# Kernel optimization log

Hardware: AMD Instinct MI355X
Metric: run time of the kernel (lower is better)

Reference implementation:

```python
import jax, jax.numpy as jnp
import numpy as np

DIM = 768
H = 12
D = DIM // H  # head_dim = 64
SCALE = D ** -0.5


def _split_heads(x):
    # [b, n, h*d] -> [b, h, n, d]
    b, n, _ = x.shape
    return x.reshape(b, n, H, D).transpose(0, 2, 1, 3)


def setup_inputs() -> dict:
    key = jax.random.key(0)
    ks = jax.random.split(key, 16)
    B, NQ, NKV = 2, 2048, 2048
    w_init = lambda k: jax.random.normal(k, (DIM, DIM), dtype=jnp.float32) * 0.02
    return {
        "words": jax.random.normal(ks[0], (B, NQ, DIM), dtype=jnp.float32),
        "position_words": jax.random.normal(ks[1], (B, NQ, DIM), dtype=jnp.float32),
        "conscious_words": jax.random.normal(ks[2], (B, NQ, DIM), dtype=jnp.float32),
        "cross_kv": jax.random.normal(ks[3], (B, NKV, DIM), dtype=jnp.float32),
        "position_cross": jax.random.normal(ks[4], (B, NKV, DIM), dtype=jnp.float32),
        "Wq_w": w_init(ks[5]), "Wk_w": w_init(ks[6]), "Wv_w": w_init(ks[7]),
        "Wq_p": w_init(ks[8]), "Wk_p": w_init(ks[9]),
        "Wq_c": w_init(ks[10]), "Wk_c": w_init(ks[11]),
        "latent_k": jax.random.normal(ks[12], (DIM,), dtype=jnp.float32),
        "Wo": w_init(ks[13]),
        "bo": jnp.zeros((DIM,), dtype=jnp.float32),
    }


def reference(words, position_words, conscious_words, cross_kv, position_cross,
              Wq_w, Wk_w, Wv_w, Wq_p, Wk_p, Wq_c, Wk_c, latent_k, Wo, bo):
    # Queries from three sources. Sum of the 9 pairwise QK^T scores equals
    # (sum of Qs) @ (sum of Ks)^T by bilinearity of matmul (same math as source).
    q = _split_heads(words @ Wq_w) + _split_heads(position_words @ Wq_p) \
        + _split_heads(conscious_words @ Wq_c)        # [b,h,nq,d]
    # latent conscious key: same vector for every kv position
    kc = (latent_k @ Wk_c).reshape(H, D)              # [h,d]
    k = _split_heads(cross_kv @ Wk_w) + _split_heads(position_cross @ Wk_p) \
        + kc[None, :, None, :]                        # [b,h,nkv,d]
    v = _split_heads(cross_kv @ Wv_w)                 # [b,h,nkv,d]

    score = jnp.einsum('bhid,bhjd->bhij', q, k) * SCALE  # [b,h,nq,nkv]
    attn = jax.nn.softmax(score, axis=-1)
    out = jnp.einsum('bhij,bhjd->bhid', attn, v)      # [b,h,nq,d]
    b, _, nq, _ = out.shape
    out = out.transpose(0, 2, 1, 3).reshape(b, nq, H * D)
    return out @ Wo + bo
```

## Files before the change

kernel.cpp:

```cpp
#include <hip/hip_runtime.h>
#include <math.h>

#define DIM  768
#define NH   12
#define HD   64
#define NQ   2048
#define NKV  2048
#define QSC_LOG2E 0.18033688011112042f

typedef short bf16x8  __attribute__((ext_vector_type(8)));
typedef float f32x4   __attribute__((ext_vector_type(4)));
typedef float f32x16  __attribute__((ext_vector_type(16)));

__device__ __forceinline__ unsigned short f2bf(float f) {
    unsigned u = __float_as_uint(f);
    unsigned r = (u + 0x7FFFu + ((u >> 16) & 1u)) >> 16;
    return (unsigned short)r;
}

__device__ __forceinline__ unsigned cvtpk_bf16(float a, float b) {
    unsigned r;
    asm("v_cvt_pk_bf16_f32 %0, %1, %2" : "=v"(r) : "v"(a), "v"(b));
    return r;
}

__device__ __forceinline__ void plswap(unsigned& a, unsigned& b) {
    asm("v_permlane32_swap_b32 %0, %1" : "+v"(a), "+v"(b));
}

__device__ __forceinline__ float vexp2f(float x) {
#if __has_builtin(__builtin_amdgcn_exp2f)
    return __builtin_amdgcn_exp2f(x);
#else
    float r;
    asm("v_exp_f32 %0, %1\ns_nop 0" : "=v"(r) : "v"(x));
    return r;
#endif
}

__device__ __forceinline__ void ld_lds16(void* lds, const void* g) {
    __builtin_amdgcn_global_load_lds(
        (const __attribute__((address_space(1))) unsigned int*)g,
        (__attribute__((address_space(3))) unsigned int*)lds, 16, 0, 0);
}

__device__ __forceinline__ f32x16 z16() {
    f32x16 r;
    #pragma unroll
    for (int e = 0; e < 16; ++e) r[e] = 0.f;
    return r;
}

union PB16 { unsigned u[4]; bf16x8 v; };

__global__ __launch_bounds__(256)
void kc2_kernel(const float* __restrict__ latent, const float* __restrict__ Wkc,
                float* __restrict__ kc) {
    __shared__ float red[16][17];
    int tx = threadIdx.x & 15, ty = threadIdx.x >> 4;
    int j = blockIdx.x * 16 + tx;
    float acc = 0.f;
    for (int i = ty * 48; i < ty * 48 + 48; ++i) acc += latent[i] * Wkc[i * DIM + j];
    red[ty][tx] = acc;
    __syncthreads();
    if (ty == 0) {
        float s = 0.f;
        #pragma unroll
        for (int k = 0; k < 16; ++k) s += red[k][tx];
        kc[j] = s;
    }
}

__global__ __launch_bounds__(256)
void convert_acts(const float* __restrict__ s0, const float* __restrict__ s1,
                  const float* __restrict__ s2, const float* __restrict__ s3,
                  const float* __restrict__ s4,
                  unsigned short* __restrict__ dstA, unsigned short* __restrict__ dstB) {
    const float* srcs[5] = {s0, s1, s2, s3, s4};
    int y = blockIdx.y;
    const float* s = srcs[y];
    unsigned short* d = (y < 4) ? (dstA + (size_t)y * 3145728) : dstB;
    size_t i = ((size_t)blockIdx.x * 256 + threadIdx.x) * 4;
    float4 v = *(const float4*)(s + i);
    ushort4 o;
    o.x = f2bf(v.x); o.y = f2bf(v.y); o.z = f2bf(v.z); o.w = f2bf(v.w);
    *(ushort4*)(d + i) = o;
}

__global__ __launch_bounds__(256)
void conv_w(const float* __restrict__ w0, const float* __restrict__ w1,
            const float* __restrict__ w2, const float* __restrict__ w3,
            const float* __restrict__ w4, const float* __restrict__ w5,
            const float* __restrict__ w6, unsigned short* __restrict__ dst) {
    __shared__ float t[32][33];
    const float* Ws[7] = {w0, w1, w2, w3, w4, w5, w6};
    const float* W = Ws[blockIdx.z];
    unsigned short* D = dst + (size_t)blockIdx.z * (768 * 768);
    int r0 = blockIdx.y * 32, c0 = blockIdx.x * 32;
    int tx = threadIdx.x & 31, ty = threadIdx.x >> 5;
    #pragma unroll
    for (int yy = 0; yy < 4; ++yy)
        t[ty * 4 + yy][tx] = W[(size_t)(r0 + ty * 4 + yy) * 768 + c0 + tx];
    __syncthreads();
    #pragma unroll
    for (int yy = 0; yy < 4; ++yy)
        D[(size_t)(c0 + ty * 4 + yy) * 768 + r0 + tx] = f2bf(t[tx][ty * 4 + yy]);
}

template<int NPAIR, int MODE>
__global__ __launch_bounds__(256)
void mfma_gemm(const unsigned short* __restrict__ A0, const unsigned short* __restrict__ B0,
               const unsigned short* __restrict__ A1, const unsigned short* __restrict__ B1,
               const unsigned short* __restrict__ A2, const unsigned short* __restrict__ B2,
               const float* __restrict__ bias, float scale, void* __restrict__ Cout) {
    __shared__ unsigned short As[2][64 * 64];
    __shared__ unsigned short Bs[2][128 * 64];
    const int tid = threadIdx.x;
    const int w = tid >> 6, l = tid & 63, g = l >> 4, r16 = l & 15;

    int o_lin = blockIdx.x + 6 * blockIdx.y;
    int wl = (o_lin & 7) * 48 + (o_lin >> 3);
    int bx = wl % 6, by = wl / 6;
    const int n0 = bx * 128, m0 = by * 64;

    const unsigned short* Alist[3] = {A0, A1, A2};
    const unsigned short* Blist[3] = {B0, B1, B2};

    f32x4 acc[4][2];
    #pragma unroll
    for (int i = 0; i < 4; ++i)
        #pragma unroll
        for (int j = 0; j < 2; ++j) acc[i][j] = (f32x4){0.f, 0.f, 0.f, 0.f};

#define GSTAGE(BUFI, AP, BP, K0) { \
    _Pragma("unroll") \
    for (int is = 0; is < 2; ++is) { \
        int u = is * 256 + tid, r = u >> 3, cc = u & 7; \
        int col = ((cc ^ (r & 7)) << 3); \
        ld_lds16((char*)As[BUFI] + is * 4096 + w * 1024, \
                 (AP) + (size_t)(m0 + r) * 768 + (K0) + col); } \
    _Pragma("unroll") \
    for (int is = 0; is < 4; ++is) { \
        int u = is * 256 + tid, r = u >> 3, cc = u & 7; \
        int col = ((cc ^ (r & 7)) << 3); \
        ld_lds16((char*)Bs[BUFI] + is * 4096 + w * 1024, \
                 (BP) + (size_t)(n0 + r) * 768 + (K0) + col); } }

    const int NSTEPS = NPAIR * 12;
    int pn = 0, kn = 0;
    GSTAGE(0, Alist[0], Blist[0], 0);
    kn = 64; if (kn == 768) { kn = 0; ++pn; }
    __syncthreads();

    #pragma unroll 1
    for (int st = 0; st < NSTEPS; ++st) {
        int cur = st & 1;
        if (st + 1 < NSTEPS) {
            GSTAGE(cur ^ 1, Alist[pn], Blist[pn], kn);
            kn += 64; if (kn == 768) { kn = 0; ++pn; }
        }
        const char* Ab = (const char*)As[cur];
        const char* Bb = (const char*)Bs[cur];
        #pragma unroll
        for (int kk = 0; kk < 2; ++kk) {
            bf16x8 af[4], bf[2];
            #pragma unroll
            for (int i = 0; i < 4; ++i) {
                int row = i * 16 + r16;
                af[i] = *(const bf16x8*)(Ab + row * 128 +
                          ((kk * 64 + g * 16) ^ ((row & 7) << 4)));
            }
            #pragma unroll
            for (int j = 0; j < 2; ++j) {
                int row = w * 32 + j * 16 + r16;
                bf[j] = *(const bf16x8*)(Bb + row * 128 +
                          ((kk * 64 + g * 16) ^ ((row & 7) << 4)));
            }
            #pragma unroll
            for (int i = 0; i < 4; ++i)
                #pragma unroll
                for (int j = 0; j < 2; ++j)
                    acc[i][j] = __builtin_amdgcn_mfma_f32_16x16x32_bf16(
                        af[i], bf[j], acc[i][j], 0, 0, 0);
        }
        __syncthreads();
    }
#undef GSTAGE

    #pragma unroll
    for (int i = 0; i < 4; ++i) {
        #pragma unroll
        for (int j = 0; j < 2; ++j) {
            int col = n0 + w * 32 + j * 16 + r16;
            float bv = ((MODE == 0 && bias) || MODE == 1) ? bias[col] : 0.f;
            #pragma unroll
            for (int rr = 0; rr < 4; ++rr) {
                int row = m0 + i * 16 + g * 4 + rr;
                float v = acc[i][j][rr];
                if (MODE == 2) v *= scale;
                v += bv;
                if (MODE == 1) {
                    ((float*)Cout)[(size_t)row * 768 + col] = v;
                } else if (MODE == 3) {
                    int bb = row >> 11, q = row & 2047;
                    ((unsigned short*)Cout)[(size_t)(bb * 768 + col) * 2048 + q] = f2bf(v);
                } else {
                    ((unsigned short*)Cout)[(size_t)row * 768 + col] = f2bf(v);
                }
            }
        }
    }
}

__global__ __launch_bounds__(256)
void flash2(const unsigned short* __restrict__ Qb,
            const unsigned short* __restrict__ Kb,
            const unsigned short* __restrict__ Vt,
            unsigned short* __restrict__ AO) {
    __shared__ unsigned short KV[2][2][4096];
    const int tid = threadIdx.x;
    const int w = tid >> 6, l = tid & 63, lo = l & 31, hi = l >> 5;

    int o_lin = blockIdx.x + 16 * blockIdx.y;
    int wl = (o_lin & 7) * 48 + (o_lin >> 3);
    int qi = wl & 15, bh = wl >> 4;
    int b = bh / NH, h = bh % NH;
    int q0 = qi * 128;

    bf16x8 qf[4];
    {
        const unsigned short* Qrow =
            Qb + (size_t)(b * NQ + q0 + w * 32 + lo) * DIM + h * HD + hi * 8;
        #pragma unroll
        for (int kc = 0; kc < 4; ++kc) qf[kc] = *(const bf16x8*)(Qrow + kc * 16);
    }

    f32x16 o0 = z16(), o1 = z16();
    float m = -3.0e38f, lsum = 0.f;

    const unsigned short* Kbase = Kb + (size_t)(b * NKV) * DIM + h * HD;
    const unsigned short* Vbase = Vt + ((size_t)b * DIM + h * HD) * NKV;

#define FSTAGE(BUFI, T0) { \
    _Pragma("unroll") \
    for (int is = 0; is < 2; ++is) { \
        int u = is * 256 + tid, r = u >> 3, cc = u & 7; \
        int col = ((cc ^ (r & 7)) << 3); \
        ld_lds16((char*)KV[BUFI][0] + is * 4096 + w * 1024, \
                 Kbase + (size_t)((T0) + r) * 768 + col); \
        ld_lds16((char*)KV[BUFI][1] + is * 4096 + w * 1024, \
                 Vbase + (size_t)r * 2048 + (T0) + col); } }

    FSTAGE(0, 0);
    __syncthreads();

    #pragma unroll 1
    for (int t = 0; t < 32; ++t) {
        int cur = t & 1;
        if (t < 31) FSTAGE(cur ^ 1, (t + 1) * 64);

        const char* Kp = (const char*)KV[cur][0];
        const char* Vp = (const char*)KV[cur][1];

        f32x16 s0 = z16(), s1 = z16();
        #pragma unroll
        for (int kc = 0; kc < 4; ++kc) {
            int r0 = lo, r1 = 32 + lo;
            bf16x8 k0 = *(const bf16x8*)(Kp + r0 * 128 +
                          ((kc * 32 + hi * 16) ^ ((r0 & 7) << 4)));
            bf16x8 k1 = *(const bf16x8*)(Kp + r1 * 128 +
                          ((kc * 32 + hi * 16) ^ ((r1 & 7) << 4)));
            s0 = __builtin_amdgcn_mfma_f32_32x32x16_bf16(k0, qf[kc], s0, 0, 0, 0);
            s1 = __builtin_amdgcn_mfma_f32_32x32x16_bf16(k1, qf[kc], s1, 0, 0, 0);
        }

        float a8[8];
        #pragma unroll
        for (int e = 0; e < 8; ++e)
            a8[e] = fmaxf(fmaxf(s0[e], s0[e + 8]), fmaxf(s1[e], s1[e + 8]));
        #pragma unroll
        for (int e = 0; e < 4; ++e) a8[e] = fmaxf(a8[e], a8[e + 4]);
        float pm = fmaxf(fmaxf(a8[0], a8[1]), fmaxf(a8[2], a8[3]));
        pm = fmaxf(pm, __shfl_xor(pm, 32));

        if (__any(pm > m + 10.f)) {
            float mn = fmaxf(m, pm);
            float sc = vexp2f(m - mn);
            lsum *= sc;
            #pragma unroll
            for (int e = 0; e < 16; ++e) { o0[e] *= sc; o1[e] *= sc; }
            m = mn;
        }

        #pragma unroll
        for (int e = 0; e < 16; ++e) {
            s0[e] = vexp2f(s0[e] - m);
            s1[e] = vexp2f(s1[e] - m);
        }

        float b8[8];
        #pragma unroll
        for (int e = 0; e < 8; ++e)
            b8[e] = (s0[e] + s0[e + 8]) + (s1[e] + s1[e + 8]);
        float rs = ((b8[0] + b8[1]) + (b8[2] + b8[3])) +
                   ((b8[4] + b8[5]) + (b8[6] + b8[7]));
        rs += __shfl_xor(rs, 32);
        lsum += rs;

        PB16 pb[4];
        #pragma unroll
        for (int cc = 0; cc < 2; ++cc) {
            unsigned a0 = cvtpk_bf16(s0[cc * 8 + 0], s0[cc * 8 + 1]);
            unsigned a1 = cvtpk_bf16(s0[cc * 8 + 2], s0[cc * 8 + 3]);
            unsigned b0 = cvtpk_bf16(s0[cc * 8 + 4], s0[cc * 8 + 5]);
            unsigned b1 = cvtpk_bf16(s0[cc * 8 + 6], s0[cc * 8 + 7]);
            plswap(a0, b0);
            plswap(a1, b1);
            pb[cc].u[0] = a0; pb[cc].u[1] = a1; pb[cc].u[2] = b0; pb[cc].u[3] = b1;
            unsigned c0 = cvtpk_bf16(s1[cc * 8 + 0], s1[cc * 8 + 1]);
            unsigned c1 = cvtpk_bf16(s1[cc * 8 + 2], s1[cc * 8 + 3]);
            unsigned d0 = cvtpk_bf16(s1[cc * 8 + 4], s1[cc * 8 + 5]);
            unsigned d1 = cvtpk_bf16(s1[cc * 8 + 6], s1[cc * 8 + 7]);
            plswap(c0, d0);
            plswap(c1, d1);
            pb[2 + cc].u[0] = c0; pb[2 + cc].u[1] = c1;
            pb[2 + cc].u[2] = d0; pb[2 + cc].u[3] = d1;
        }

        #pragma unroll
        for (int c = 0; c < 4; ++c) {
            int r0 = lo, r1 = 32 + lo;
            bf16x8 v0 = *(const bf16x8*)(Vp + r0 * 128 +
                          ((c * 32 + hi * 16) ^ ((r0 & 7) << 4)));
            bf16x8 v1 = *(const bf16x8*)(Vp + r1 * 128 +
                          ((c * 32 + hi * 16) ^ ((r1 & 7) << 4)));
            o0 = __builtin_amdgcn_mfma_f32_32x32x16_bf16(v0, pb[c].v, o0, 0, 0, 0);
            o1 = __builtin_amdgcn_mfma_f32_32x32x16_bf16(v1, pb[c].v, o1, 0, 0, 0);
        }
        __syncthreads();
    }
#undef FSTAGE

    float inv = 1.f / lsum;
    char* eb = (char*)KV + w * 4096;
    #pragma unroll
    for (int r = 0; r < 16; r += 2) {
        int d0 = (r & 3) + 8 * (r >> 2) + 4 * hi;
        *(unsigned*)(eb + lo * 128 + ((2 * d0) ^ ((lo & 7) << 4))) =
            cvtpk_bf16(o0[r] * inv, o0[r + 1] * inv);
        int d1 = 32 + d0;
        *(unsigned*)(eb + lo * 128 + ((2 * d1) ^ ((lo & 7) << 4))) =
            cvtpk_bf16(o1[r] * inv, o1[r + 1] * inv);
    }
    int q2 = l >> 1, h2 = l & 1;
    size_t grow = (size_t)(b * NQ + q0 + w * 32 + q2) * DIM + h * HD + h2 * 32;
    #pragma unroll
    for (int c = 0; c < 4; ++c) {
        uint4 vv = *(const uint4*)(eb + q2 * 128 + ((h2 * 64 + c * 16) ^ ((q2 & 7) << 4)));
        *(uint4*)(AO + grow + c * 8) = vv;
    }
}

extern "C" void kernel_launch(void* const* d_in, const int* in_sizes, int n_in,
                              void* d_out, int out_size, void* d_ws, size_t ws_size,
                              hipStream_t stream) {
    const float* words   = (const float*)d_in[0];
    const float* posw    = (const float*)d_in[1];
    const float* consc   = (const float*)d_in[2];
    const float* cross   = (const float*)d_in[3];
    const float* pcross  = (const float*)d_in[4];
    const float* Wq_w    = (const float*)d_in[5];
    const float* Wk_w    = (const float*)d_in[6];
    const float* Wv_w    = (const float*)d_in[7];
    const float* Wq_p    = (const float*)d_in[8];
    const float* Wk_p    = (const float*)d_in[9];
    const float* Wq_c    = (const float*)d_in[10];
    const float* Wk_c    = (const float*)d_in[11];
    const float* latentk = (const float*)d_in[12];
    const float* Wo      = (const float*)d_in[13];
    const float* bo      = (const float*)d_in[14];

    char* arena = (char*)d_ws;
    const size_t ACTB = 6291456;
    unsigned short* act0 = (unsigned short*)(arena);
    unsigned short* act1 = (unsigned short*)(arena + ACTB);
    unsigned short* act2 = (unsigned short*)(arena + 2 * ACTB);
    unsigned short* act3 = (unsigned short*)(arena + 3 * ACTB);
    unsigned short* wt   = (unsigned short*)(arena + 4 * ACTB);
    const size_t WTE = 768 * 768;
    unsigned short* qb  = (unsigned short*)(arena + 4 * ACTB + 7 * WTE * 2);
    unsigned short* pcb = (unsigned short*)((char*)qb + ACTB);
    float* kcv          = (float*)((char*)pcb + ACTB);

    unsigned short* kb = act1;
    unsigned short* vt = act2;
    unsigned short* ao = act0;

    convert_acts<<<dim3(3072, 5), dim3(256), 0, stream>>>(
        words, posw, consc, cross, pcross, act0, pcb);
    conv_w<<<dim3(24, 24, 7), dim3(256), 0, stream>>>(
        Wq_w, Wq_p, Wq_c, Wk_w, Wk_p, Wv_w, Wo, wt);
    kc2_kernel<<<dim3(48), dim3(256), 0, stream>>>(latentk, Wk_c, kcv);

    mfma_gemm<3, 2><<<dim3(6, 64), dim3(256), 0, stream>>>(
        act0, wt + 0 * WTE, act1, wt + 1 * WTE, act2, wt + 2 * WTE,
        nullptr, QSC_LOG2E, qb);
    mfma_gemm<1, 3><<<dim3(6, 64), dim3(256), 0, stream>>>(
        act3, wt + 5 * WTE, nullptr, nullptr, nullptr, nullptr,
        nullptr, 1.f, vt);
    mfma_gemm<2, 0><<<dim3(6, 64), dim3(256), 0, stream>>>(
        act3, wt + 3 * WTE, pcb, wt + 4 * WTE, nullptr, nullptr,
        kcv, 1.f, kb);
    flash2<<<dim3(16, 24), dim3(256), 0, stream>>>(qb, kb, vt, ao);
    mfma_gemm<1, 1><<<dim3(6, 64), dim3(256), 0, stream>>>(
        ao, wt + 6 * WTE, nullptr, nullptr, nullptr, nullptr,
        bo, 1.f, (float*)d_out);
}
```

Before: 160.0 us.

## Split attention KV range in two with combine pass, merge Q/V projection launches

The flash attention kernel now splits each (batch, head, q-tile) over two halves of the KV sequence. That doubles the grid from 384 to 768 blocks for better CU occupancy. Each half writes unnormalized partial outputs plus running max and sum, and a new combine kernel merges them into the attention output. The Q and V projection GEMMs are fused into one launch through a runtime-configured GEMM kernel, and workspace buffers are reused. The cost is extra global traffic for the partial outputs, an extra launch, and runtime mode branches that replace template constants in the GEMM.

```diff
diff --git a/kernel.cpp b/kernel.cpp
--- a/kernel.cpp
+++ b/kernel.cpp
@@ -16,6 +16,9 @@
     unsigned u = __float_as_uint(f);
     unsigned r = (u + 0x7FFFu + ((u >> 16) & 1u)) >> 16;
     return (unsigned short)r;
+}
+__device__ __forceinline__ float bf2f(unsigned short u) {
+    return __uint_as_float(((unsigned)u) << 16);
 }
 
 __device__ __forceinline__ unsigned cvtpk_bf16(float a, float b) {
@@ -74,12 +77,11 @@
 __global__ __launch_bounds__(256)
 void convert_acts(const float* __restrict__ s0, const float* __restrict__ s1,
                   const float* __restrict__ s2, const float* __restrict__ s3,
-                  const float* __restrict__ s4,
-                  unsigned short* __restrict__ dstA, unsigned short* __restrict__ dstB) {
-    const float* srcs[5] = {s0, s1, s2, s3, s4};
+                  unsigned short* __restrict__ dstA) {
+    const float* srcs[4] = {s0, s1, s2, s3};
     int y = blockIdx.y;
     const float* s = srcs[y];
-    unsigned short* d = (y < 4) ? (dstA + (size_t)y * 3145728) : dstB;
+    unsigned short* d = dstA + (size_t)y * 3145728;
     size_t i = ((size_t)blockIdx.x * 256 + threadIdx.x) * 4;
     float4 v = *(const float4*)(s + i);
     ushort4 o;
@@ -107,24 +109,40 @@
         D[(size_t)(c0 + ty * 4 + yy) * 768 + r0 + tx] = f2bf(t[tx][ty * 4 + yy]);
 }
 
-template<int NPAIR, int MODE>
-__global__ __launch_bounds__(256)
-void mfma_gemm(const unsigned short* __restrict__ A0, const unsigned short* __restrict__ B0,
-               const unsigned short* __restrict__ A1, const unsigned short* __restrict__ B1,
-               const unsigned short* __restrict__ A2, const unsigned short* __restrict__ B2,
-               const float* __restrict__ bias, float scale, void* __restrict__ Cout) {
+struct GemmCfg {
+    const unsigned short* A0; const unsigned short* A1; const unsigned short* A2;
+    const unsigned short* B0; const unsigned short* B1; const unsigned short* B2;
+    const float* bias; float scale; void* out; int npair; int mode;
+};
+
+__global__ __launch_bounds__(256)
+void gemm_any(GemmCfg c0, GemmCfg c1, int nblk) {
     __shared__ unsigned short As[2][64 * 64];
     __shared__ unsigned short Bs[2][128 * 64];
     const int tid = threadIdx.x;
     const int w = tid >> 6, l = tid & 63, g = l >> 4, r16 = l & 15;
 
-    int o_lin = blockIdx.x + 6 * blockIdx.y;
-    int wl = (o_lin & 7) * 48 + (o_lin >> 3);
-    int bx = wl % 6, by = wl / 6;
+    int o_lin = blockIdx.x + 6 * blockIdx.y + 384 * blockIdx.z;
+    int per = nblk >> 3;
+    int wl = (o_lin & 7) * per + (o_lin >> 3);
+    int zz = wl / 384, rem = wl - zz * 384;
+    int bx = rem % 6, by = rem / 6;
     const int n0 = bx * 128, m0 = by * 64;
 
-    const unsigned short* Alist[3] = {A0, A1, A2};
-    const unsigned short* Blist[3] = {B0, B1, B2};
+    const unsigned short* Alist[3];
+    const unsigned short* Blist[3];
+    const float* bias; float scale; void* Cout; int npair, mode;
+    if (zz == 0) {
+        Alist[0] = c0.A0; Alist[1] = c0.A1; Alist[2] = c0.A2;
+        Blist[0] = c0.B0; Blist[1] = c0.B1; Blist[2] = c0.B2;
+        bias = c0.bias; scale = c0.scale; Cout = c0.out;
+        npair = c0.npair; mode = c0.mode;
+    } else {
+        Alist[0] = c1.A0; Alist[1] = c1.A1; Alist[2] = c1.A2;
+        Blist[0] = c1.B0; Blist[1] = c1.B1; Blist[2] = c1.B2;
+        bias = c1.bias; scale = c1.scale; Cout = c1.out;
+        npair = c1.npair; mode = c1.mode;
+    }
 
     f32x4 acc[4][2];
     #pragma unroll
@@ -146,10 +164,10 @@
         ld_lds16((char*)Bs[BUFI] + is * 4096 + w * 1024, \
                  (BP) + (size_t)(n0 + r) * 768 + (K0) + col); } }
 
-    const int NSTEPS = NPAIR * 12;
+    const int NSTEPS = npair * 12;
     int pn = 0, kn = 0;
     GSTAGE(0, Alist[0], Blist[0], 0);
-    kn = 64; if (kn == 768) { kn = 0; ++pn; }
+    kn = 64;
     __syncthreads();
 
     #pragma unroll 1
@@ -192,16 +210,16 @@
         #pragma unroll
         for (int j = 0; j < 2; ++j) {
             int col = n0 + w * 32 + j * 16 + r16;
-            float bv = ((MODE == 0 && bias) || MODE == 1) ? bias[col] : 0.f;
+            float bv = ((mode == 0 && bias) || mode == 1) ? bias[col] : 0.f;
             #pragma unroll
             for (int rr = 0; rr < 4; ++rr) {
                 int row = m0 + i * 16 + g * 4 + rr;
                 float v = acc[i][j][rr];
-                if (MODE == 2) v *= scale;
+                if (mode == 2) v *= scale;
                 v += bv;
-                if (MODE == 1) {
+                if (mode == 1) {
                     ((float*)Cout)[(size_t)row * 768 + col] = v;
-                } else if (MODE == 3) {
+                } else if (mode == 3) {
                     int bb = row >> 11, q = row & 2047;
                     ((unsigned short*)Cout)[(size_t)(bb * 768 + col) * 2048 + q] = f2bf(v);
                 } else {
@@ -216,16 +234,19 @@
 void flash2(const unsigned short* __restrict__ Qb,
             const unsigned short* __restrict__ Kb,
             const unsigned short* __restrict__ Vt,
-            unsigned short* __restrict__ AO) {
+            unsigned short* __restrict__ P0,
+            unsigned short* __restrict__ P1,
+            float2* __restrict__ ML) {
     __shared__ unsigned short KV[2][2][4096];
     const int tid = threadIdx.x;
     const int w = tid >> 6, l = tid & 63, lo = l & 31, hi = l >> 5;
 
-    int o_lin = blockIdx.x + 16 * blockIdx.y;
-    int wl = (o_lin & 7) * 48 + (o_lin >> 3);
-    int qi = wl & 15, bh = wl >> 4;
+    int o_lin = blockIdx.x + 32 * blockIdx.y;
+    int wl = (o_lin & 7) * 96 + (o_lin >> 3);
+    int qi = wl & 15, part = (wl >> 4) & 1, bh = wl >> 5;
     int b = bh / NH, h = bh % NH;
     int q0 = qi * 128;
+    int kvbase = part * 1024;
 
     bf16x8 qf[4];
     {
@@ -251,13 +272,13 @@
         ld_lds16((char*)KV[BUFI][1] + is * 4096 + w * 1024, \
                  Vbase + (size_t)r * 2048 + (T0) + col); } }
 
-    FSTAGE(0, 0);
+    FSTAGE(0, kvbase);
     __syncthreads();
 
     #pragma unroll 1
-    for (int t = 0; t < 32; ++t) {
+    for (int t = 0; t < 16; ++t) {
         int cur = t & 1;
-        if (t < 31) FSTAGE(cur ^ 1, (t + 1) * 64);
+        if (t < 15) FSTAGE(cur ^ 1, kvbase + (t + 1) * 64);
 
         const char* Kp = (const char*)KV[cur][0];
         const char* Vp = (const char*)KV[cur][1];
@@ -341,23 +362,46 @@
     }
 #undef FSTAGE
 
-    float inv = 1.f / lsum;
-    char* eb = (char*)KV + w * 4096;
-    #pragma unroll
-    for (int r = 0; r < 16; r += 2) {
+    unsigned short* Op = (part ? P1 : P0) + (size_t)bh * 64 * 2048;
+    int q = q0 + w * 32 + lo;
+    #pragma unroll
+    for (int r = 0; r < 16; ++r) {
         int d0 = (r & 3) + 8 * (r >> 2) + 4 * hi;
-        *(unsigned*)(eb + lo * 128 + ((2 * d0) ^ ((lo & 7) << 4))) =
-            cvtpk_bf16(o0[r] * inv, o0[r + 1] * inv);
-        int d1 = 32 + d0;
-        *(unsigned*)(eb + lo * 128 + ((2 * d1) ^ ((lo & 7) << 4))) =
-            cvtpk_bf16(o1[r] * inv, o1[r + 1] * inv);
-    }
-    int q2 = l >> 1, h2 = l & 1;
-    size_t grow = (size_t)(b * NQ + q0 + w * 32 + q2) * DIM + h * HD + h2 * 32;
-    #pragma unroll
-    for (int c = 0; c < 4; ++c) {
-        uint4 vv = *(const uint4*)(eb + q2 * 128 + ((h2 * 64 + c * 16) ^ ((q2 & 7) << 4)));
-        *(uint4*)(AO + grow + c * 8) = vv;
+        Op[(size_t)d0 * 2048 + q] = f2bf(o0[r]);
+        Op[(size_t)(32 + d0) * 2048 + q] = f2bf(o1[r]);
+    }
+    if (hi == 0)
+        ML[(size_t)(part * 24 + bh) * 2048 + q] = make_float2(m, lsum);
+}
+
+__global__ __launch_bounds__(256)
+void combine_kernel(const unsigned short* __restrict__ P0,
+                    const unsigned short* __restrict__ P1,
+                    const float2* __restrict__ ML,
+                    unsigned short* __restrict__ AO) {
+    int bh = blockIdx.y;
+    int q = blockIdx.x * 256 + threadIdx.x;
+    float2 u0 = ML[(size_t)bh * 2048 + q];
+    float2 u1 = ML[(size_t)(24 + bh) * 2048 + q];
+    float M = fmaxf(u0.x, u1.x);
+    float w0 = vexp2f(u0.x - M), w1 = vexp2f(u1.x - M);
+    float inv = 1.f / (w0 * u0.y + w1 * u1.y);
+    w0 *= inv; w1 *= inv;
+    int b = bh / NH, h = bh % NH;
+    const unsigned short* p0 = P0 + (size_t)bh * 64 * 2048 + q;
+    const unsigned short* p1 = P1 + (size_t)bh * 64 * 2048 + q;
+    unsigned short* dst = AO + ((size_t)(b * 2048 + q)) * DIM + h * HD;
+    #pragma unroll
+    for (int dc = 0; dc < 8; ++dc) {
+        unsigned rr[4];
+        #pragma unroll
+        for (int e = 0; e < 4; ++e) {
+            int d = dc * 8 + e * 2;
+            float v0 = w0 * bf2f(p0[(size_t)d * 2048]) + w1 * bf2f(p1[(size_t)d * 2048]);
+            float v1 = w0 * bf2f(p0[(size_t)(d + 1) * 2048]) + w1 * bf2f(p1[(size_t)(d + 1) * 2048]);
+            rr[e] = cvtpk_bf16(v0, v1);
+        }
+        *(uint4*)(dst + dc * 8) = make_uint4(rr[0], rr[1], rr[2], rr[3]);
     }
 }
 
@@ -382,37 +426,40 @@
 
     char* arena = (char*)d_ws;
     const size_t ACTB = 6291456;
-    unsigned short* act0 = (unsigned short*)(arena);
-    unsigned short* act1 = (unsigned short*)(arena + ACTB);
-    unsigned short* act2 = (unsigned short*)(arena + 2 * ACTB);
-    unsigned short* act3 = (unsigned short*)(arena + 3 * ACTB);
-    unsigned short* wt   = (unsigned short*)(arena + 4 * ACTB);
-    const size_t WTE = 768 * 768;
-    unsigned short* qb  = (unsigned short*)(arena + 4 * ACTB + 7 * WTE * 2);
-    unsigned short* pcb = (unsigned short*)((char*)qb + ACTB);
-    float* kcv          = (float*)((char*)pcb + ACTB);
-
-    unsigned short* kb = act1;
-    unsigned short* vt = act2;
-    unsigned short* ao = act0;
-
-    convert_acts<<<dim3(3072, 5), dim3(256), 0, stream>>>(
-        words, posw, consc, cross, pcross, act0, pcb);
+    const size_t WTE  = 768 * 768;
+    unsigned short* S0 = (unsigned short*)(arena);
+    unsigned short* S1 = (unsigned short*)(arena + ACTB);
+    unsigned short* S2 = (unsigned short*)(arena + 2 * ACTB);
+    unsigned short* S3 = (unsigned short*)(arena + 3 * ACTB);
+    unsigned short* WT = (unsigned short*)(arena + 4 * ACTB);
+    unsigned short* QB = WT + 7 * WTE;
+    unsigned short* VT = (unsigned short*)((char*)QB + ACTB);
+    float* KCV         = (float*)((char*)VT + ACTB);
+
+    float2* ML = (float2*)S3;
+
+    convert_acts<<<dim3(3072, 4), dim3(256), 0, stream>>>(words, posw, consc, cross, S0);
     conv_w<<<dim3(24, 24, 7), dim3(256), 0, stream>>>(
-        Wq_w, Wq_p, Wq_c, Wk_w, Wk_p, Wv_w, Wo, wt);
-    kc2_kernel<<<dim3(48), dim3(256), 0, stream>>>(latentk, Wk_c, kcv);
-
-    mfma_gemm<3, 2><<<dim3(6, 64), dim3(256), 0, stream>>>(
-        act0, wt + 0 * WTE, act1, wt + 1 * WTE, act2, wt + 2 * WTE,
-        nullptr, QSC_LOG2E, qb);
-    mfma_gemm<1, 3><<<dim3(6, 64), dim3(256), 0, stream>>>(
-        act3, wt + 5 * WTE, nullptr, nullptr, nullptr, nullptr,
-        nullptr, 1.f, vt);
-    mfma_gemm<2, 0><<<dim3(6, 64), dim3(256), 0, stream>>>(
-        act3, wt + 3 * WTE, pcb, wt + 4 * WTE, nullptr, nullptr,
-        kcv, 1.f, kb);
-    flash2<<<dim3(16, 24), dim3(256), 0, stream>>>(qb, kb, vt, ao);
-    mfma_gemm<1, 1><<<dim3(6, 64), dim3(256), 0, stream>>>(
-        ao, wt + 6 * WTE, nullptr, nullptr, nullptr, nullptr,
-        bo, 1.f, (float*)d_out);
-}
+        Wq_w, Wq_p, Wq_c, Wk_w, Wk_p, Wv_w, Wo, WT);
+    kc2_kernel<<<dim3(48), dim3(256), 0, stream>>>(latentk, Wk_c, KCV);
+
+    GemmCfg cq = { S0, S1, S2, WT + 0 * WTE, WT + 1 * WTE, WT + 2 * WTE,
+                   nullptr, QSC_LOG2E, QB, 3, 2 };
+    GemmCfg cv = { S3, nullptr, nullptr, WT + 5 * WTE, nullptr, nullptr,
+                   nullptr, 1.f, VT, 1, 3 };
+    gemm_any<<<dim3(6, 64, 2), dim3(256), 0, stream>>>(cq, cv, 768);
+
+    convert_acts<<<dim3(3072, 1), dim3(256), 0, stream>>>(pcross, nullptr, nullptr, nullptr, S0);
+
+    GemmCfg ck = { S3, S0, nullptr, WT + 3 * WTE, WT + 4 * WTE, nullptr,
+                   KCV, 1.f, S1, 2, 0 };
+    gemm_any<<<dim3(6, 64, 1), dim3(256), 0, stream>>>(ck, ck, 384);
+
+    flash2<<<dim3(32, 24), dim3(256), 0, stream>>>(QB, S1, VT, S2, S0, ML);
+
+    combine_kernel<<<dim3(8, 24), dim3(256), 0, stream>>>(S2, S0, ML, QB);
+
+    GemmCfg co = { QB, nullptr, nullptr, WT + 6 * WTE, nullptr, nullptr,
+                   bo, 1.f, (float*)d_out, 1, 1 };
+    gemm_any<<<dim3(6, 64, 1), dim3(256), 0, stream>>>(co, co, 384);
+}
```

Measured after the change: 160.8 us. No clear change (+0.5%).
